# Performance work log

Measured on AMD Instinct MI355X. Metric: run time of the kernel, lower is better.

Reference implementation:

```python
import jax, jax.numpy as jnp
import numpy as np

N, L, F, C, H, D = 2, 512, 128, 64, 12, 16
INF = 1e5
SQ29 = float(np.sqrt(2.0 / 9.0))
SCALE = float(np.sqrt(1.0 / 3.0))
EPS_DIR = 1e-4
LN_EPS = 1e-5


def setup_inputs() -> dict:
    key = jax.random.key(0)
    ks = jax.random.split(key, 16)
    s = 0.02
    return {
        "R": jax.random.normal(ks[0], (N, L, 3, 3), jnp.float32),
        "t": jax.random.normal(ks[1], (N, L, 3), jnp.float32),
        "p_CB": jax.random.normal(ks[2], (N, L, 3), jnp.float32),
        "x": jax.random.normal(ks[3], (N, L, F), jnp.float32),
        "z": jax.random.normal(ks[4], (N, L, L, C), jnp.float32),
        "mask": jax.random.randint(ks[5], (N, L), 0, 2).astype(bool),
        "Wq": jax.random.normal(ks[6], (H * D, F), jnp.float32) * s,
        "Wk": jax.random.normal(ks[7], (H * D, F), jnp.float32) * s,
        "Wv": jax.random.normal(ks[8], (H * D, F), jnp.float32) * s,
        "Wpb": jax.random.normal(ks[9], (H, C), jnp.float32) * s,
        "gamma_raw": jnp.full((1, 1, 1, H), float(np.log(np.e - 1.0)), jnp.float32),
        "Wout": jax.random.normal(ks[10], (F, H * C + H * D + H * 7), jnp.float32) * s,
        "bout": jnp.zeros((F,), jnp.float32),
        "ln_w": jnp.ones((F,), jnp.float32),
        "ln_b": jnp.zeros((F,), jnp.float32),
    }


def reference(R, t, p_CB, x, z, mask, Wq, Wk, Wv, Wpb, gamma_raw, Wout, bout, ln_w, ln_b):
    # --- logits ---
    q = (x @ Wq.T).reshape(N, L, H, D)  # (N,L,H,D)
    k = (x @ Wk.T).reshape(N, L, H, D)
    v = (x @ Wv.T).reshape(N, L, H, D)
    logits_node = jnp.einsum('nihd,njhd->nijh', q, k)
    logits_pair = jnp.einsum('nijc,hc->nijh', z, Wpb)
    # CB squared distances, identical for all heads -> broadcast over H
    d2 = jnp.sum((p_CB[:, :, None, :] - p_CB[:, None, :, :]) ** 2, axis=-1)[..., None]  # (N,L,L,1)
    gamma = jax.nn.softplus(gamma_raw)  # (1,1,1,H)
    logits_beta = d2 * (-gamma * SQ29 / 2.0)
    logits = (logits_node + logits_pair + logits_beta) * SCALE
    # --- masked softmax over axis j (2) ---
    mask_row = mask[:, :, None, None]
    mask_pair = mask_row & mask[:, None, :, None]
    logits = jnp.where(mask_pair, logits, logits - INF)
    alpha = jax.nn.softmax(logits, axis=2)
    alpha = jnp.where(mask_row, alpha, jnp.zeros_like(alpha))  # (N,L,L,H)
    # --- pair aggregation ---
    feat_p2n = jnp.einsum('nijh,nijc->nihc', alpha, z).reshape(N, L, H * C)
    # --- node aggregation ---
    feat_node = jnp.einsum('nijh,njhd->nihd', alpha, v).reshape(N, L, H * D)
    # --- beta (CB point) aggregation ---
    aggr = jnp.einsum('nijh,njc->nihc', alpha, p_CB)  # (N,L,H,3) in global frame
    local = jnp.einsum('nlji,nlhj->nlhi', R, aggr - t[:, :, None, :])  # global_to_local: R^T (q - t)
    dist = jnp.linalg.norm(local, axis=-1)  # (N,L,H)
    direction = local / (dist[..., None] + EPS_DIR)
    feat_spatial = jnp.concatenate(
        [local.reshape(N, L, -1), dist.reshape(N, L, -1), direction.reshape(N, L, -1)], axis=-1)
    # --- output transform + residual layernorm ---
    feat_all = jnp.concatenate([feat_p2n, feat_node, feat_spatial], axis=-1) @ Wout.T + bout
    feat_all = jnp.where(mask[:, :, None], feat_all, 0.0)
    y = x + feat_all
    mu = jnp.mean(y, axis=-1, keepdims=True)
    var = jnp.var(y, axis=-1, keepdims=True)
    return (y - mu) / jnp.sqrt(var + LN_EPS) * ln_w + ln_b
```

## Files before the change

kernel.cpp:

```cpp
#include <hip/hip_runtime.h>
#include <hip/hip_bf16.h>

constexpr int NB   = 2;
constexpr int LL   = 512;
constexpr int LLP  = 516;
constexpr int FF   = 128;
constexpr int CC   = 64;
constexpr int HH   = 12;
constexpr int DD   = 16;
constexpr int HD   = HH * DD;
constexpr int FEAT = HH*CC + HH*DD + HH*7;
constexpr float INFV   = 100000.0f;
constexpr float SCALEF = 0.57735026918962576f;
constexpr float SQ29H  = 0.23570226039551584f;

__global__ void compact_kernel(const int* __restrict__ maskg, int* __restrict__ row_map)
{
    const int tid = threadIdx.x;
    const int lane = tid & 63, wv = tid >> 6;
    __shared__ int s_cnt[16];
    __shared__ int s_off[16];
    __shared__ int s_tot;
    const int m = maskg[tid] ? 1 : 0;
    unsigned long long b = __ballot(m);
    const int pre = __popcll(b & ((1ull << lane) - 1ull));
    if (lane == 0) s_cnt[wv] = __popcll(b);
    __syncthreads();
    if (tid == 0) {
        int s = 0;
        for (int w = 0; w < 16; ++w) { s_off[w] = s; s += s_cnt[w]; }
        s_tot = s;
    }
    __syncthreads();
    const int nact = s_off[wv] + pre;
    if (m) row_map[nact] = tid;
    else   row_map[s_tot + (tid - nact)] = tid;
}

__global__ __launch_bounds__(192) void qkv_kernel(
    const float* __restrict__ xg, const float* __restrict__ Wq,
    const float* __restrict__ Wk, const float* __restrict__ Wv,
    float* __restrict__ q_ws, float* __restrict__ kT4, float* __restrict__ vT)
{
    const int b = blockIdx.x;
    const int t = threadIdx.x;
    __shared__ __align__(16) float sx[4*FF];
    __shared__ __align__(16) float sw[3*HD*20];

    for (int o = t; o < 4*FF; o += 192) sx[o] = xg[(size_t)b*4*FF + o];

    float aq[4] = {0.f,0.f,0.f,0.f};
    float ak[4] = {0.f,0.f,0.f,0.f};
    float av[4] = {0.f,0.f,0.f,0.f};

    for (int ft = 0; ft < 8; ++ft) {
        __syncthreads();
        #pragma unroll
        for (int m = 0; m < 3; ++m) {
            const float* W = (m == 0) ? Wq : ((m == 1) ? Wk : Wv);
            #pragma unroll
            for (int p = 0; p < 4; ++p) {
                const int r = (t >> 2) + 48*p, q = t & 3;
                float4 v = *(const float4*)(W + (size_t)r*FF + ft*16 + q*4);
                *(float4*)&sw[m*3840 + r*20 + q*4] = v;
            }
        }
        __syncthreads();
        const float* wq = &sw[0*3840 + t*20];
        const float* wk = &sw[1*3840 + t*20];
        const float* wv = &sw[2*3840 + t*20];
        #pragma unroll
        for (int f4 = 0; f4 < 4; ++f4) {
            float4 a  = *(const float4*)&wq[f4*4];
            float4 bq = *(const float4*)&wk[f4*4];
            float4 cq = *(const float4*)&wv[f4*4];
            #pragma unroll
            for (int r = 0; r < 4; ++r) {
                float4 xv = *(const float4*)&sx[r*FF + ft*16 + f4*4];
                aq[r] += xv.x*a.x  + xv.y*a.y  + xv.z*a.z  + xv.w*a.w;
                ak[r] += xv.x*bq.x + xv.y*bq.y + xv.z*bq.z + xv.w*bq.w;
                av[r] += xv.x*cq.x + xv.y*cq.y + xv.z*cq.z + xv.w*cq.w;
            }
        }
    }
    const int n = (b*4) >> 9, i0 = (b*4) & 511;
    #pragma unroll
    for (int r = 0; r < 4; ++r) {
        const int row = b*4 + r, i = i0 + r;
        q_ws[(size_t)row*HD + t] = aq[r];
        kT4[(((size_t)n*48 + (t >> 2))*LL + i)*4 + (t & 3)] = ak[r];
    }
    *(float4*)&vT[((size_t)n*HD + t)*LL + i0] = make_float4(av[0], av[1], av[2], av[3]);
}

__global__ __launch_bounds__(512, 2) void attn_kernel(
    const float* __restrict__ Rg, const float* __restrict__ tg, const float* __restrict__ pg,
    const float* __restrict__ xg, const float* __restrict__ zg, const int* __restrict__ maskg,
    const float* __restrict__ Wpbg, const float* __restrict__ gammag,
    const float* __restrict__ Woutg, const float* __restrict__ boutg,
    const float* __restrict__ lnwg, const float* __restrict__ lnbg,
    const float* __restrict__ q_ws, const float* __restrict__ kT4, const float* __restrict__ vT,
    const int* __restrict__ row_map, float* __restrict__ outg)
{
    const int row = row_map[blockIdx.x];
    const int n = row >> 9;
    const int tid = threadIdx.x;

    __shared__ __align__(16) float s_exp[HH*LLP];
    __shared__ __align__(16) float s_big[4*768];
    __shared__ __align__(16) float s_p[3*LL];
    __shared__ __align__(16) float s_q[HD];
    __shared__ __align__(16) float s_x[FF];
    __shared__ __align__(16) float s_y[FF];
    __shared__ __align__(16) float s_f[FEAT];
    __shared__ float s_aggr[36];
    __shared__ float s_inv[HH];
    __shared__ float s_coef[HH];
    __shared__ float s_geo[15];
    __shared__ float s_red[2];

    if (tid < FF) s_x[tid] = xg[(size_t)row*FF + tid];
    if (tid >= 128 && tid < 128 + HD) s_q[tid-128] = q_ws[(size_t)row*HD + (tid-128)];
    for (int o = tid; o < HH*CC; o += 512) s_big[o] = Wpbg[o];
    for (int o = tid; o < 3*LL; o += 512) s_p[o] = pg[(size_t)n*3*LL + o];
    if (tid >= 320 && tid < 332) {
        float g = gammag[tid-320];
        float gamma = log1pf(__expf(fminf(g, 80.0f)));
        s_coef[tid-320] = -gamma * SQ29H;
    }
    if (tid >= 332 && tid < 335) s_geo[tid-332] = pg[(size_t)row*3 + (tid-332)];
    if (tid >= 335 && tid < 338) s_geo[3 + tid-335] = tg[(size_t)row*3 + (tid-335)];
    if (tid >= 338 && tid < 347) s_geo[6 + tid-338] = Rg[(size_t)row*9 + (tid-338)];
    const int mi = maskg[row];
    __syncthreads();

    if (mi) {
        {
            const int j = tid;
            float acc[HH];
            #pragma unroll
            for (int h = 0; h < HH; ++h) acc[h] = 0.f;

            const float* zr = zg + ((size_t)row*LL + j)*CC;
            float4 zv[16];
            #pragma unroll
            for (int c4 = 0; c4 < 16; ++c4) zv[c4] = ((const float4*)zr)[c4];
            #pragma unroll
            for (int c4 = 0; c4 < 16; ++c4) {
                #pragma unroll
                for (int h = 0; h < HH; ++h) {
                    float4 w = *(const float4*)&s_big[h*CC + c4*4];
                    acc[h] += zv[c4].x*w.x + zv[c4].y*w.y + zv[c4].z*w.z + zv[c4].w*w.w;
                }
            }
            const float* kb = kT4 + ((size_t)(n*48)*LL + j)*4;
            #pragma unroll
            for (int g = 0; g < 6; ++g) {
                float4 kv[8];
                #pragma unroll
                for (int u = 0; u < 8; ++u)
                    kv[u] = *(const float4*)(kb + (size_t)(g*8+u)*LL*4);
                #pragma unroll
                for (int u = 0; u < 8; ++u) {
                    const int hd4 = g*8+u;
                    float4 q4v = *(const float4*)&s_q[hd4*4];
                    acc[hd4 >> 2] += q4v.x*kv[u].x + q4v.y*kv[u].y + q4v.z*kv[u].z + q4v.w*kv[u].w;
                }
            }
            float e0 = s_geo[0]-s_p[j*3+0];
            float e1 = s_geo[1]-s_p[j*3+1];
            float e2 = s_geo[2]-s_p[j*3+2];
            float d2 = e0*e0 + e1*e1 + e2*e2;
            const float sub = maskg[n*LL + j] ? 0.0f : INFV;
            #pragma unroll
            for (int h = 0; h < HH; ++h) {
                float lg = (acc[h] + d2*s_coef[h]) * SCALEF - sub;
                s_exp[h*LLP + j] = __expf(fminf(lg, 80.0f));
            }
        }
        __syncthreads();

        {
            const int wv = tid >> 6, lane = tid & 63;
            for (int h = wv; h < HH; h += 8) {
                float s = 0.f;
                #pragma unroll
                for (int r = 0; r < 8; ++r) s += s_exp[h*LLP + lane + (r<<6)];
                #pragma unroll
                for (int off = 32; off > 0; off >>= 1) s += __shfl_xor(s, off, 64);
                if (lane == 0) s_inv[h] = 1.0f / fmaxf(s, 1e-30f);
            }
        }
        __syncthreads();

        {
            const int wv = tid >> 6, lane = tid & 63;
            if (wv < 4) {
                const int c = lane, q4v = wv;
                float acc[HH];
                #pragma unroll
                for (int h = 0; h < HH; ++h) acc[h] = 0.f;
                const float* zb = zg + ((size_t)row*LL + q4v*128)*CC + c;
                const float* ep = s_exp + q4v*128;
                #pragma unroll 2
                for (int jj = 0; jj < 128; jj += 8) {
                    float z0 = zb[(size_t)(jj+0)*CC];
                    float z1 = zb[(size_t)(jj+1)*CC];
                    float z2 = zb[(size_t)(jj+2)*CC];
                    float z3 = zb[(size_t)(jj+3)*CC];
                    float z4 = zb[(size_t)(jj+4)*CC];
                    float z5 = zb[(size_t)(jj+5)*CC];
                    float z6 = zb[(size_t)(jj+6)*CC];
                    float z7 = zb[(size_t)(jj+7)*CC];
                    #pragma unroll
                    for (int h = 0; h < HH; ++h) {
                        float4 ea = *(const float4*)&ep[h*LLP + jj];
                        float4 eb = *(const float4*)&ep[h*LLP + jj + 4];
                        acc[h] += ea.x*z0 + ea.y*z1 + ea.z*z2 + ea.w*z3
                                + eb.x*z4 + eb.y*z5 + eb.z*z6 + eb.w*z7;
                    }
                }
                #pragma unroll
                for (int h = 0; h < HH; ++h) s_big[q4v*768 + h*64 + c] = acc[h];
            } else if (tid < 448) {
                const int hd = tid - 256;
                const float* vb = vT + ((size_t)n*HD + hd)*LL;
                const float* ep = s_exp + (hd >> 4)*LLP;
                float a = 0.f;
                #pragma unroll 2
                for (int j4 = 0; j4 < 128; j4 += 4) {
                    float4 v0 = *(const float4*)(vb + j4*4);
                    float4 v1 = *(const float4*)(vb + j4*4 + 4);
                    float4 v2 = *(const float4*)(vb + j4*4 + 8);
                    float4 v3 = *(const float4*)(vb + j4*4 + 12);
                    float4 e0 = *(const float4*)(ep + j4*4);
                    float4 e1 = *(const float4*)(ep + j4*4 + 4);
                    float4 e2 = *(const float4*)(ep + j4*4 + 8);
                    float4 e3 = *(const float4*)(ep + j4*4 + 12);
                    a += v0.x*e0.x + v0.y*e0.y + v0.z*e0.z + v0.w*e0.w
                       + v1.x*e1.x + v1.y*e1.y + v1.z*e1.z + v1.w*e1.w
                       + v2.x*e2.x + v2.y*e2.y + v2.z*e2.z + v2.w*e2.w
                       + v3.x*e3.x + v3.y*e3.y + v3.z*e3.z + v3.w*e3.w;
                }
                s_f[768 + hd] = a * s_inv[hd >> 4];
            } else {
                const int o = tid - 448;
                if (o < 36) {
                    const int h = o / 3, ax = o - h*3;
                    const float* ep = s_exp + h*LLP;
                    float a = 0.f;
                    #pragma unroll 8
                    for (int j = 0; j < LL; ++j) a += ep[j] * s_p[j*3 + ax];
                    s_aggr[o] = a * s_inv[h];
                }
            }
        }
        __syncthreads();

        for (int o = tid; o < 768; o += 512)
            s_f[o] = (s_big[o] + s_big[768+o] + s_big[1536+o] + s_big[2304+o]) * s_inv[o >> 6];
        if (tid >= 500) {
            const int h = tid - 500;
            float m0 = s_aggr[h*3+0] - s_geo[3];
            float m1 = s_aggr[h*3+1] - s_geo[4];
            float m2 = s_aggr[h*3+2] - s_geo[5];
            const float* Rm = &s_geo[6];
            float l0 = Rm[0]*m0 + Rm[3]*m1 + Rm[6]*m2;
            float l1 = Rm[1]*m0 + Rm[4]*m1 + Rm[7]*m2;
            float l2 = Rm[2]*m0 + Rm[5]*m1 + Rm[8]*m2;
            float dist = sqrtf(l0*l0 + l1*l1 + l2*l2);
            float idn = 1.0f/(dist + 1e-4f);
            s_f[960 + h*3+0] = l0; s_f[960 + h*3+1] = l1; s_f[960 + h*3+2] = l2;
            s_f[996 + h] = dist;
            s_f[1008 + h*3+0] = l0*idn; s_f[1008 + h*3+1] = l1*idn; s_f[1008 + h*3+2] = l2*idn;
        }
        __syncthreads();

        {
            const int f = tid & 127, q4 = tid >> 7;
            const float* wr = Woutg + (size_t)f * FEAT;
            float acc = 0.f;
            #pragma unroll 4
            for (int kk = q4*4; kk < FEAT; kk += 16) {
                float4 fv  = *(const float4*)&s_f[kk];
                float4 wvv = *(const float4*)(wr + kk);
                acc += fv.x*wvv.x + fv.y*wvv.y + fv.z*wvv.z + fv.w*wvv.w;
            }
            s_big[q4*FF + f] = acc;
        }
        __syncthreads();
        if (tid < FF)
            s_y[tid] = s_x[tid] + boutg[tid]
                     + s_big[tid] + s_big[FF + tid] + s_big[2*FF + tid] + s_big[3*FF + tid];
    } else {
        if (tid < FF) s_y[tid] = s_x[tid];
    }
    __syncthreads();

    if (tid < 64) {
        float a = s_y[tid], b = s_y[tid + 64];
        float s1 = a + b, s2 = a*a + b*b;
        #pragma unroll
        for (int off = 32; off > 0; off >>= 1) {
            s1 += __shfl_xor(s1, off, 64);
            s2 += __shfl_xor(s2, off, 64);
        }
        if (tid == 0) { s_red[0] = s1; s_red[1] = s2; }
    }
    __syncthreads();
    if (tid < FF) {
        float mu  = s_red[0] * (1.0f/FF);
        float var = s_red[1] * (1.0f/FF) - mu*mu;
        float vv = (s_y[tid] - mu) * rsqrtf(fmaxf(var, 0.0f) + 1e-5f);
        vv = vv * lnwg[tid] + lnbg[tid];
        outg[(size_t)row*FF + tid] = vv;
    }
}

extern "C" void kernel_launch(void* const* d_in, const int* in_sizes, int n_in,
                              void* d_out, int out_size, void* d_ws, size_t ws_size,
                              hipStream_t stream) {
    const float* Rg    = (const float*)d_in[0];
    const float* tg    = (const float*)d_in[1];
    const float* pg    = (const float*)d_in[2];
    const float* xg    = (const float*)d_in[3];
    const float* zg    = (const float*)d_in[4];
    const int*   maskg = (const int*)d_in[5];
    const float* Wq    = (const float*)d_in[6];
    const float* Wk    = (const float*)d_in[7];
    const float* Wv    = (const float*)d_in[8];
    const float* Wpb   = (const float*)d_in[9];
    const float* gam   = (const float*)d_in[10];
    const float* Wout  = (const float*)d_in[11];
    const float* bout  = (const float*)d_in[12];
    const float* lnw   = (const float*)d_in[13];
    const float* lnb   = (const float*)d_in[14];
    float* outp = (float*)d_out;

    float* q_ws = (float*)d_ws;
    float* kT4  = q_ws + (size_t)NB*LL*HD;
    float* vT   = kT4  + (size_t)NB*LL*HD;
    int*   row_map = (int*)(vT + (size_t)NB*LL*HD);

    compact_kernel<<<1, NB*LL, 0, stream>>>(maskg, row_map);
    qkv_kernel<<<NB*LL/4, HD, 0, stream>>>(xg, Wq, Wk, Wv, q_ws, kT4, vT);
    attn_kernel<<<NB*LL, 512, 0, stream>>>(Rg, tg, pg, xg, zg, maskg,
                                           Wpb, gam, Wout, bout, lnw, lnb,
                                           q_ws, kT4, vT, row_map, outp);
}
```

Before: 294.9 us.

## Defer softmax normalization, read Wpb from global, and reduce Wout partials via shuffles

The pair-bias weights are now read directly from global memory (uniform, cacheable loads) instead of being staged into shared memory. The row-sum reduction is folded into the idle wave of the aggregation phase, and normalization is applied afterwards, which removes one block barrier. The output projection maps four adjacent lanes to one feature and combines them with wavefront shuffles instead of a shared-memory round trip, removing another barrier. The trade-off is that the last wave serially reduces all 12 heads, and the Wout reads become strided per lane.

```diff
diff --git a/kernel.cpp b/kernel.cpp
--- a/kernel.cpp
+++ b/kernel.cpp
@@ -121,7 +121,6 @@
 
     if (tid < FF) s_x[tid] = xg[(size_t)row*FF + tid];
     if (tid >= 128 && tid < 128 + HD) s_q[tid-128] = q_ws[(size_t)row*HD + (tid-128)];
-    for (int o = tid; o < HH*CC; o += 512) s_big[o] = Wpbg[o];
     for (int o = tid; o < 3*LL; o += 512) s_p[o] = pg[(size_t)n*3*LL + o];
     if (tid >= 320 && tid < 332) {
         float g = gammag[tid-320];
@@ -138,20 +137,21 @@
         {
             const int j = tid;
             float acc[HH];
-            #pragma unroll
-            for (int h = 0; h < HH; ++h) acc[h] = 0.f;
 
             const float* zr = zg + ((size_t)row*LL + j)*CC;
             float4 zv[16];
             #pragma unroll
             for (int c4 = 0; c4 < 16; ++c4) zv[c4] = ((const float4*)zr)[c4];
             #pragma unroll
-            for (int c4 = 0; c4 < 16; ++c4) {
-                #pragma unroll
-                for (int h = 0; h < HH; ++h) {
-                    float4 w = *(const float4*)&s_big[h*CC + c4*4];
-                    acc[h] += zv[c4].x*w.x + zv[c4].y*w.y + zv[c4].z*w.z + zv[c4].w*w.w;
-                }
+            for (int h = 0; h < HH; ++h) {
+                const float4* wh = (const float4*)(Wpbg + h*CC);
+                float a = 0.f;
+                #pragma unroll
+                for (int c4 = 0; c4 < 16; ++c4) {
+                    float4 w = wh[c4];
+                    a += zv[c4].x*w.x + zv[c4].y*w.y + zv[c4].z*w.z + zv[c4].w*w.w;
+                }
+                acc[h] = a;
             }
             const float* kb = kT4 + ((size_t)(n*48)*LL + j)*4;
             #pragma unroll
@@ -176,19 +176,6 @@
             for (int h = 0; h < HH; ++h) {
                 float lg = (acc[h] + d2*s_coef[h]) * SCALEF - sub;
                 s_exp[h*LLP + j] = __expf(fminf(lg, 80.0f));
-            }
-        }
-        __syncthreads();
-
-        {
-            const int wv = tid >> 6, lane = tid & 63;
-            for (int h = wv; h < HH; h += 8) {
-                float s = 0.f;
-                #pragma unroll
-                for (int r = 0; r < 8; ++r) s += s_exp[h*LLP + lane + (r<<6)];
-                #pragma unroll
-                for (int off = 32; off > 0; off >>= 1) s += __shfl_xor(s, off, 64);
-                if (lane == 0) s_inv[h] = 1.0f / fmaxf(s, 1e-30f);
             }
         }
         __syncthreads();
@@ -242,28 +229,41 @@
                        + v2.x*e2.x + v2.y*e2.y + v2.z*e2.z + v2.w*e2.w
                        + v3.x*e3.x + v3.y*e3.y + v3.z*e3.z + v3.w*e3.w;
                 }
-                s_f[768 + hd] = a * s_inv[hd >> 4];
+                s_f[768 + hd] = a;
             } else {
                 const int o = tid - 448;
+                for (int h = 0; h < HH; ++h) {
+                    float s = 0.f;
+                    #pragma unroll
+                    for (int r = 0; r < 8; ++r) s += s_exp[h*LLP + lane + (r<<6)];
+                    #pragma unroll
+                    for (int off = 32; off > 0; off >>= 1) s += __shfl_xor(s, off, 64);
+                    if (lane == 0) s_inv[h] = 1.0f / fmaxf(s, 1e-30f);
+                }
                 if (o < 36) {
                     const int h = o / 3, ax = o - h*3;
                     const float* ep = s_exp + h*LLP;
                     float a = 0.f;
                     #pragma unroll 8
                     for (int j = 0; j < LL; ++j) a += ep[j] * s_p[j*3 + ax];
-                    s_aggr[o] = a * s_inv[h];
-                }
-            }
-        }
-        __syncthreads();
-
-        for (int o = tid; o < 768; o += 512)
-            s_f[o] = (s_big[o] + s_big[768+o] + s_big[1536+o] + s_big[2304+o]) * s_inv[o >> 6];
+                    s_aggr[o] = a;
+                }
+            }
+        }
+        __syncthreads();
+
+        for (int o = tid; o < 960; o += 512) {
+            if (o < 768)
+                s_f[o] = (s_big[o] + s_big[768+o] + s_big[1536+o] + s_big[2304+o]) * s_inv[o >> 6];
+            else
+                s_f[o] = s_f[o] * s_inv[(o - 768) >> 4];
+        }
         if (tid >= 500) {
             const int h = tid - 500;
-            float m0 = s_aggr[h*3+0] - s_geo[3];
-            float m1 = s_aggr[h*3+1] - s_geo[4];
-            float m2 = s_aggr[h*3+2] - s_geo[5];
+            const float iv = s_inv[h];
+            float m0 = s_aggr[h*3+0]*iv - s_geo[3];
+            float m1 = s_aggr[h*3+1]*iv - s_geo[4];
+            float m2 = s_aggr[h*3+2]*iv - s_geo[5];
             const float* Rm = &s_geo[6];
             float l0 = Rm[0]*m0 + Rm[3]*m1 + Rm[6]*m2;
             float l1 = Rm[1]*m0 + Rm[4]*m1 + Rm[7]*m2;
@@ -277,7 +277,7 @@
         __syncthreads();
 
         {
-            const int f = tid & 127, q4 = tid >> 7;
+            const int f = tid >> 2, q4 = tid & 3;
             const float* wr = Woutg + (size_t)f * FEAT;
             float acc = 0.f;
             #pragma unroll 4
@@ -286,12 +286,10 @@
                 float4 wvv = *(const float4*)(wr + kk);
                 acc += fv.x*wvv.x + fv.y*wvv.y + fv.z*wvv.z + fv.w*wvv.w;
             }
-            s_big[q4*FF + f] = acc;
-        }
-        __syncthreads();
-        if (tid < FF)
-            s_y[tid] = s_x[tid] + boutg[tid]
-                     + s_big[tid] + s_big[FF + tid] + s_big[2*FF + tid] + s_big[3*FF + tid];
+            acc += __shfl_xor(acc, 1, 64);
+            acc += __shfl_xor(acc, 2, 64);
+            if (q4 == 0) s_y[f] = s_x[f] + boutg[f] + acc;
+        }
     } else {
         if (tid < FF) s_y[tid] = s_x[tid];
     }
```

Measured after the change: 272.1 us. 7.7% less time.
